# Optimization experiments

Hardware: AMD Instinct MI355X
Metric: run time of the kernel (lower is better)

## Reference

```python
import jax, jax.numpy as jnp
import numpy as np

B, S, D, H = 4, 2048, 1024, 16
HD = D // H  # head dim = 64


def setup_inputs() -> dict:
    key = jax.random.key(0)
    ks = jax.random.split(key, 10)
    scale = 1.0 / np.sqrt(D)
    return {
        "query": jax.random.normal(ks[0], (B, S, D), jnp.float32),
        "key": jax.random.normal(ks[1], (B, S, D), jnp.float32),
        "value": jax.random.normal(ks[2], (B, S, D), jnp.float32),
        "mask": jnp.zeros((B, 1, 1, S), jnp.bool_),  # True = masked out
        "Wq": jax.random.normal(ks[3], (D, D), jnp.float32) * scale,
        "bq": jnp.zeros((D,), jnp.float32),
        "Wk": jax.random.normal(ks[4], (D, D), jnp.float32) * scale,
        "bk": jnp.zeros((D,), jnp.float32),
        "Wv": jax.random.normal(ks[5], (D, D), jnp.float32) * scale,
        "bv": jnp.zeros((D,), jnp.float32),
    }


def reference(query, key, value, mask, Wq, bq, Wk, bk, Wv, bv):
    # QKV projections, then split heads: [B,S,D] -> [B,H,S,HD]
    def split_heads(x):
        return x.reshape(B, S, H, HD).transpose(0, 2, 1, 3)

    q = split_heads(query @ Wq + bq)
    k = split_heads(key @ Wk + bk)
    v = split_heads(value @ Wv + bv)

    inv_sqrt_d = jnp.float32(1.0 / np.sqrt(HD))
    scores = jnp.einsum("bhqd,bhkd->bhqk", q, k) * inv_sqrt_d  # [B,H,S,S]
    # Source semantics: tf.where(mask == False, scores, -inf) -> mask True is masked
    scores = jnp.where(mask, -jnp.inf, scores)
    attn = jax.nn.softmax(scores, axis=-1)
    out = jnp.einsum("bhqk,bhkd->bhqd", attn, v)  # [B,H,S,HD]
    # merge heads back to [B,S,D]; source forward() omits the output projection
    return out.transpose(0, 2, 1, 3).reshape(B, S, D)
```

## Files before the change

kernel.cpp:

```cpp
#include <hip/hip_runtime.h>
#include <hip/hip_bf16.h>
#include <stdint.h>


#define Bn 4
#define Sn 2048
#define Dn 1024
#define Hn 16
#define HDn 64

typedef __attribute__((ext_vector_type(8))) short short8;
typedef __attribute__((ext_vector_type(4))) float f32x4;
typedef __attribute__((ext_vector_type(4))) int i32x4;

__device__ __forceinline__ unsigned short f2b(float f) {
  __hip_bfloat16 h = __float2bfloat16(f);
  return __builtin_bit_cast(unsigned short, h);
}

__device__ __forceinline__ float fexp2(float x) {
#if __has_builtin(__builtin_amdgcn_exp2f)
  return __builtin_amdgcn_exp2f(x);
#else
  float r;
  asm("v_exp_f32 %0, %1" : "=v"(r) : "v"(x));
  return r;
#endif
}

__device__ __forceinline__ uint32_t cvtpk(float lo, float hi) {
  uint32_t r;
  asm("v_cvt_pk_bf16_f32 %0, %1, %2" : "=v"(r) : "v"(lo), "v"(hi));
  return r;
}

__device__ __forceinline__ void gload_lds16(const void* g, void* l) {
  __builtin_amdgcn_global_load_lds(
      (const __attribute__((address_space(1))) unsigned int*)(uintptr_t)g,
      (__attribute__((address_space(3))) unsigned int*)(uint32_t)(uintptr_t)l,
      16, 0, 0);
}

__global__ __launch_bounds__(256) void wt_kernel(const float* __restrict__ W,
                                                 unsigned short* __restrict__ Wt) {
  __shared__ float tile[32][33];
  const int k0 = blockIdx.x * 32, n0 = blockIdx.y * 32;
  const int tx = threadIdx.x, ty = threadIdx.y;
  #pragma unroll
  for (int j = 0; j < 32; j += 8)
    tile[ty + j][tx] = W[(size_t)(k0 + ty + j) * Dn + n0 + tx];
  __syncthreads();
  #pragma unroll
  for (int j = 0; j < 32; j += 8)
    Wt[(size_t)(n0 + ty + j) * Dn + k0 + tx] = f2b(tile[tx][ty + j]);
}

__global__ __launch_bounds__(256) void proj_gemm(const float* __restrict__ X,
                                                 const unsigned short* __restrict__ Wt,
                                                 const float* __restrict__ bias,
                                                 unsigned short* __restrict__ out,
                                                 int vt_mode) {
  __shared__ __align__(16) unsigned short Asm[128 * 32];
  __shared__ __align__(16) unsigned short Bsm[128 * 32];
  const int tid = threadIdx.x;
  const int wave = tid >> 6, lane = tid & 63;
  const int c = lane & 15, g = lane >> 4;
  const int m0 = blockIdx.x * 128, n0 = blockIdx.y * 128;
  const int wm = (wave >> 1) * 64, wn = (wave & 1) * 64;

  f32x4 acc[4][4];
  #pragma unroll
  for (int i = 0; i < 4; i++)
    #pragma unroll
    for (int j = 0; j < 4; j++) acc[i][j] = (f32x4){0.f, 0.f, 0.f, 0.f};

  for (int kt = 0; kt < Dn / 32; ++kt) {
    const int k0 = kt * 32;
    #pragma unroll
    for (int iss = 0; iss < 2; ++iss) {
      int idx = iss * 256 + tid;
      int r = idx >> 2, c8 = idx & 3;
      gload_lds16(Wt + (size_t)(n0 + r) * Dn + k0 + c8 * 8, &Bsm[idx * 8]);
    }
    #pragma unroll
    for (int iss = 0; iss < 2; ++iss) {
      int idx = iss * 256 + tid;
      int r = idx >> 2, c8 = idx & 3;
      const float* src = X + (size_t)(m0 + r) * Dn + k0 + c8 * 8;
      float4 v0 = *(const float4*)src;
      float4 v1 = *(const float4*)(src + 4);
      short8 pk;
      pk[0] = (short)f2b(v0.x); pk[1] = (short)f2b(v0.y);
      pk[2] = (short)f2b(v0.z); pk[3] = (short)f2b(v0.w);
      pk[4] = (short)f2b(v1.x); pk[5] = (short)f2b(v1.y);
      pk[6] = (short)f2b(v1.z); pk[7] = (short)f2b(v1.w);
      *(short8*)&Asm[idx * 8] = pk;
    }
    __syncthreads();

    short8 af[4], bfr[4];
    #pragma unroll
    for (int mf = 0; mf < 4; ++mf)
      af[mf] = *(const short8*)&Asm[(wm + mf * 16 + c) * 32 + g * 8];
    #pragma unroll
    for (int nf = 0; nf < 4; ++nf)
      bfr[nf] = *(const short8*)&Bsm[(wn + nf * 16 + c) * 32 + g * 8];
    #pragma unroll
    for (int mf = 0; mf < 4; ++mf)
      #pragma unroll
      for (int nf = 0; nf < 4; ++nf)
        acc[mf][nf] = __builtin_amdgcn_mfma_f32_16x16x32_bf16(af[mf], bfr[nf], acc[mf][nf], 0, 0, 0);
    __syncthreads();
  }

  #pragma unroll
  for (int mf = 0; mf < 4; ++mf) {
    #pragma unroll
    for (int nf = 0; nf < 4; ++nf) {
      #pragma unroll
      for (int i = 0; i < 4; ++i) {
        int row = m0 + wm + mf * 16 + g * 4 + i;
        int col = n0 + wn + nf * 16 + c;
        float v = acc[mf][nf][i] + bias[col];
        int bb = row >> 11, srow = row & 2047;
        int hh = col >> 6, hd = col & 63;
        size_t o;
        if (!vt_mode)
          o = (((size_t)bb * Hn + hh) * Sn + srow) * HDn + hd;
        else
          o = (((size_t)bb * Hn + hh) * HDn + hd) * Sn + srow;
        out[o] = f2b(v);
      }
    }
  }
}

__global__ __launch_bounds__(256) void attn_kernel(const unsigned short* __restrict__ Qg,
                                                   const unsigned short* __restrict__ Kg,
                                                   const unsigned short* __restrict__ Vtg,
                                                   const uint8_t* __restrict__ maskg,
                                                   float* __restrict__ out) {
  __shared__ __align__(16) unsigned short Ksm[2][64 * 64];
  __shared__ __align__(16) unsigned short Vsm[2][64 * 64];
  __shared__ __align__(16) uint32_t Plds[4][16 * 32];
  __shared__ __align__(16) float biasLds[Sn];

  const int b = blockIdx.z, h = blockIdx.y;
  const int q0 = blockIdx.x * 64;
  const int tid = threadIdx.x;
  const int wave = tid >> 6, lane = tid & 63;
  const int c = lane & 15, g = lane >> 4;
  const int cs = c & 7;
  const int bh = b * Hn + h;

  const unsigned short* kbase = Kg + (size_t)bh * Sn * HDn;
  const unsigned short* vbase = Vtg + (size_t)bh * HDn * Sn;

  const unsigned short* qptr = Qg + ((size_t)bh * Sn + q0 + wave * 16 + c) * HDn;
  const short8 qf0 = *(const short8*)(qptr + g * 8);
  const short8 qf1 = *(const short8*)(qptr + 32 + g * 8);

  auto stage = [&](int t, int buf) {
    const int kv0 = t * 64;
    #pragma unroll
    for (int iss = 0; iss < 2; ++iss) {
      int idx = iss * 256 + tid;
      int r = idx >> 3, c8 = idx & 7;
      int c8s = c8 ^ (r & 7);
      gload_lds16(kbase + (size_t)(kv0 + r) * HDn + c8s * 8, &Ksm[buf][idx * 8]);
      gload_lds16(vbase + (size_t)r * Sn + kv0 + c8s * 8, &Vsm[buf][idx * 8]);
    }
  };

  stage(0, 0);

  {
    const uint8_t* mb = maskg + (size_t)b * Sn;
    uint2 w = *(const uint2*)(mb + tid * 8);
    float4 f0, f1;
    f0.x = (w.x & 0x000000ffu) ? -1e30f : 0.f;
    f0.y = (w.x & 0x0000ff00u) ? -1e30f : 0.f;
    f0.z = (w.x & 0x00ff0000u) ? -1e30f : 0.f;
    f0.w = (w.x & 0xff000000u) ? -1e30f : 0.f;
    f1.x = (w.y & 0x000000ffu) ? -1e30f : 0.f;
    f1.y = (w.y & 0x0000ff00u) ? -1e30f : 0.f;
    f1.z = (w.y & 0x00ff0000u) ? -1e30f : 0.f;
    f1.w = (w.y & 0xff000000u) ? -1e30f : 0.f;
    *(float4*)&biasLds[tid * 8] = f0;
    *(float4*)&biasLds[tid * 8 + 4] = f1;
  }
  __syncthreads();

  f32x4 O[4];
  #pragma unroll
  for (int i = 0; i < 4; i++) O[i] = (f32x4){0.f, 0.f, 0.f, 0.f};
  float m = -INFINITY, l = 0.f;

  const float SCALE = 0.125f * 1.44269504088896340736f;
  uint32_t* pw = &Plds[wave][0];

  for (int t = 0; t < Sn / 64; ++t) {
    const int cur = t & 1;
    const int kv0 = t * 64;
    if (t < Sn / 64 - 1) stage(t + 1, cur ^ 1);

    f32x4 s[4];
    #pragma unroll
    for (int cf = 0; cf < 4; ++cf) {
      const unsigned short* krow = &Ksm[cur][(cf * 16 + c) * 64];
      short8 kb0 = *(const short8*)&krow[((0 + g) ^ cs) * 8];
      short8 kb1 = *(const short8*)&krow[((4 + g) ^ cs) * 8];
      s[cf] = (f32x4){0.f, 0.f, 0.f, 0.f};
      s[cf] = __builtin_amdgcn_mfma_f32_16x16x32_bf16(kb0, qf0, s[cf], 0, 0, 0);
      s[cf] = __builtin_amdgcn_mfma_f32_16x16x32_bf16(kb1, qf1, s[cf], 0, 0, 0);
    }

    #pragma unroll
    for (int cf = 0; cf < 4; ++cf) {
      f32x4 bv = *(const f32x4*)&biasLds[kv0 + cf * 16 + g * 4];
      #pragma unroll
      for (int i = 0; i < 4; i++) s[cf][i] = s[cf][i] * SCALE + bv[i];
    }

    float pm = s[0][0];
    #pragma unroll
    for (int cf = 0; cf < 4; ++cf)
      #pragma unroll
      for (int i = 0; i < 4; i++) pm = fmaxf(pm, s[cf][i]);
    pm = fmaxf(pm, __shfl_xor(pm, 16, 64));
    pm = fmaxf(pm, __shfl_xor(pm, 32, 64));

    if (__any(pm > m + 8.0f)) {
      float mn = fmaxf(m, pm);
      float sf = fexp2(m - mn);
      m = mn;
      l *= sf;
      #pragma unroll
      for (int hf = 0; hf < 4; ++hf)
        #pragma unroll
        for (int i = 0; i < 4; i++) O[hf][i] *= sf;
    }

    float rs = 0.f;
    #pragma unroll
    for (int cf = 0; cf < 4; ++cf)
      #pragma unroll
      for (int i = 0; i < 4; i++) {
        float p = fexp2(s[cf][i] - m);
        s[cf][i] = p;
        rs += p;
      }
    rs += __shfl_xor(rs, 16, 64);
    rs += __shfl_xor(rs, 32, 64);
    l += rs;

    #pragma unroll
    for (int cf = 0; cf < 4; ++cf) {
      uint32_t w0 = cvtpk(s[cf][0], s[cf][1]);
      uint32_t w1 = cvtpk(s[cf][2], s[cf][3]);
      int base = (cf * 8 + g * 2) ^ (cs << 2);
      pw[c * 32 + base] = w0;
      pw[c * 32 + base + 1] = w1;
    }
    short8 pb0 = *(const short8*)&pw[c * 32 + ((g * 4) ^ (cs << 2))];
    short8 pb1 = *(const short8*)&pw[c * 32 + ((16 + g * 4) ^ (cs << 2))];
    #pragma unroll
    for (int hf = 0; hf < 4; ++hf) {
      const unsigned short* vrow = &Vsm[cur][(hf * 16 + c) * 64];
      short8 va0 = *(const short8*)&vrow[((0 + g) ^ cs) * 8];
      short8 va1 = *(const short8*)&vrow[((4 + g) ^ cs) * 8];
      O[hf] = __builtin_amdgcn_mfma_f32_16x16x32_bf16(va0, pb0, O[hf], 0, 0, 0);
      O[hf] = __builtin_amdgcn_mfma_f32_16x16x32_bf16(va1, pb1, O[hf], 0, 0, 0);
    }
    __syncthreads();
  }

  const float inv = 1.0f / l;
  const int q = q0 + wave * 16 + c;
  float* op = out + ((size_t)b * Sn + q) * Dn + h * HDn;
  #pragma unroll
  for (int hf = 0; hf < 4; ++hf) {
    float4 st;
    st.x = O[hf][0] * inv;
    st.y = O[hf][1] * inv;
    st.z = O[hf][2] * inv;
    st.w = O[hf][3] * inv;
    *(float4*)&op[hf * 16 + g * 4] = st;
  }
}

extern "C" void kernel_launch(void* const* d_in, const int* in_sizes, int n_in,
                              void* d_out, int out_size, void* d_ws, size_t ws_size,
                              hipStream_t stream) {
  (void)in_sizes; (void)n_in; (void)out_size; (void)ws_size;
  const float* query = (const float*)d_in[0];
  const float* key   = (const float*)d_in[1];
  const float* value = (const float*)d_in[2];
  const uint8_t* mask = (const uint8_t*)d_in[3];
  const float* Wq = (const float*)d_in[4];
  const float* bq = (const float*)d_in[5];
  const float* Wk = (const float*)d_in[6];
  const float* bk = (const float*)d_in[7];
  const float* Wv = (const float*)d_in[8];
  const float* bv = (const float*)d_in[9];
  float* out = (float*)d_out;

  unsigned short* wtq = (unsigned short*)d_ws;
  unsigned short* wtk = wtq + (size_t)Dn * Dn;
  unsigned short* wtv = wtk + (size_t)Dn * Dn;
  unsigned short* Qb  = wtv + (size_t)Dn * Dn;
  unsigned short* Kb  = Qb + (size_t)Bn * Sn * Dn;
  unsigned short* Vtb = Kb + (size_t)Bn * Sn * Dn;

  dim3 tb(32, 8);
  dim3 tg(Dn / 32, Dn / 32);
  wt_kernel<<<tg, tb, 0, stream>>>(Wq, wtq);
  wt_kernel<<<tg, tb, 0, stream>>>(Wk, wtk);
  wt_kernel<<<tg, tb, 0, stream>>>(Wv, wtv);

  dim3 gg(Bn * Sn / 128, Dn / 128);
  proj_gemm<<<gg, 256, 0, stream>>>(query, wtq, bq, Qb, 0);
  proj_gemm<<<gg, 256, 0, stream>>>(key,   wtk, bk, Kb, 0);
  proj_gemm<<<gg, 256, 0, stream>>>(value, wtv, bv, Vtb, 1);

  dim3 ag(Sn / 64, Hn, Bn);
  attn_kernel<<<ag, 256, 0, stream>>>(Qb, Kb, Vtb, mask, out);
}
```

Measured before the change: 424.6 us.

## Batch QKV launches, fold softmax scale into Q, skip bias for unmasked tiles

Merges the three weight-transpose launches and the three projection GEMMs into single launches indexed by blockIdx.z, so each stage fills the GPU with one larger grid. The softmax scale (1/sqrt(d)·log2 e) is folded into the Q projection epilogue, and bf16 conversion uses packed cvt instructions. In the attention loop a per-64-key-tile mask flag lets fully unmasked tiles skip the bias add, and the row-max is computed as a shallower reduction tree. Rounding Q to bf16 after scaling slightly changes numerics, and the flag check adds a small LDS read per tile.

```diff
diff --git a/kernel.cpp b/kernel.cpp
--- a/kernel.cpp
+++ b/kernel.cpp
@@ -8,6 +8,7 @@
 #define Dn 1024
 #define Hn 16
 #define HDn 64
+#define QSCALE (0.125f * 1.44269504088896340736f)
 
 typedef __attribute__((ext_vector_type(8))) short short8;
 typedef __attribute__((ext_vector_type(4))) float f32x4;
@@ -41,9 +42,16 @@
       16, 0, 0);
 }
 
-__global__ __launch_bounds__(256) void wt_kernel(const float* __restrict__ W,
-                                                 unsigned short* __restrict__ Wt) {
+__global__ __launch_bounds__(256) void wt3_kernel(const float* __restrict__ Wq,
+                                                  const float* __restrict__ Wk,
+                                                  const float* __restrict__ Wv,
+                                                  unsigned short* __restrict__ wtq,
+                                                  unsigned short* __restrict__ wtk,
+                                                  unsigned short* __restrict__ wtv) {
   __shared__ float tile[32][33];
+  const int z = blockIdx.z;
+  const float* W = z == 0 ? Wq : (z == 1 ? Wk : Wv);
+  unsigned short* Wt = z == 0 ? wtq : (z == 1 ? wtk : wtv);
   const int k0 = blockIdx.x * 32, n0 = blockIdx.y * 32;
   const int tx = threadIdx.x, ty = threadIdx.y;
   #pragma unroll
@@ -55,13 +63,28 @@
     Wt[(size_t)(n0 + ty + j) * Dn + k0 + tx] = f2b(tile[tx][ty + j]);
 }
 
-__global__ __launch_bounds__(256) void proj_gemm(const float* __restrict__ X,
-                                                 const unsigned short* __restrict__ Wt,
-                                                 const float* __restrict__ bias,
-                                                 unsigned short* __restrict__ out,
-                                                 int vt_mode) {
+__global__ __launch_bounds__(256) void proj3_gemm(const float* __restrict__ Xq,
+                                                  const float* __restrict__ Xk,
+                                                  const float* __restrict__ Xv,
+                                                  const unsigned short* __restrict__ wtq,
+                                                  const unsigned short* __restrict__ wtk,
+                                                  const unsigned short* __restrict__ wtv,
+                                                  const float* __restrict__ bq,
+                                                  const float* __restrict__ bk,
+                                                  const float* __restrict__ bv,
+                                                  unsigned short* __restrict__ Qb,
+                                                  unsigned short* __restrict__ Kb,
+                                                  unsigned short* __restrict__ Vtb) {
   __shared__ __align__(16) unsigned short Asm[128 * 32];
   __shared__ __align__(16) unsigned short Bsm[128 * 32];
+  const int z = blockIdx.z;
+  const float* X = z == 0 ? Xq : (z == 1 ? Xk : Xv);
+  const unsigned short* Wt = z == 0 ? wtq : (z == 1 ? wtk : wtv);
+  const float* bias = z == 0 ? bq : (z == 1 ? bk : bv);
+  unsigned short* out = z == 0 ? Qb : (z == 1 ? Kb : Vtb);
+  const float osc = z == 0 ? QSCALE : 1.0f;
+  const int vt_mode = (z == 2);
+
   const int tid = threadIdx.x;
   const int wave = tid >> 6, lane = tid & 63;
   const int c = lane & 15, g = lane >> 4;
@@ -89,12 +112,12 @@
       const float* src = X + (size_t)(m0 + r) * Dn + k0 + c8 * 8;
       float4 v0 = *(const float4*)src;
       float4 v1 = *(const float4*)(src + 4);
-      short8 pk;
-      pk[0] = (short)f2b(v0.x); pk[1] = (short)f2b(v0.y);
-      pk[2] = (short)f2b(v0.z); pk[3] = (short)f2b(v0.w);
-      pk[4] = (short)f2b(v1.x); pk[5] = (short)f2b(v1.y);
-      pk[6] = (short)f2b(v1.z); pk[7] = (short)f2b(v1.w);
-      *(short8*)&Asm[idx * 8] = pk;
+      i32x4 pk;
+      pk[0] = (int)cvtpk(v0.x, v0.y);
+      pk[1] = (int)cvtpk(v0.z, v0.w);
+      pk[2] = (int)cvtpk(v1.x, v1.y);
+      pk[3] = (int)cvtpk(v1.z, v1.w);
+      *(i32x4*)&Asm[idx * 8] = pk;
     }
     __syncthreads();
 
@@ -121,7 +144,7 @@
       for (int i = 0; i < 4; ++i) {
         int row = m0 + wm + mf * 16 + g * 4 + i;
         int col = n0 + wn + nf * 16 + c;
-        float v = acc[mf][nf][i] + bias[col];
+        float v = (acc[mf][nf][i] + bias[col]) * osc;
         int bb = row >> 11, srow = row & 2047;
         int hh = col >> 6, hd = col & 63;
         size_t o;
@@ -144,6 +167,7 @@
   __shared__ __align__(16) unsigned short Vsm[2][64 * 64];
   __shared__ __align__(16) uint32_t Plds[4][16 * 32];
   __shared__ __align__(16) float biasLds[Sn];
+  __shared__ int flagsLds[Sn / 64];
 
   const int b = blockIdx.z, h = blockIdx.y;
   const int q0 = blockIdx.x * 64;
@@ -155,6 +179,7 @@
 
   const unsigned short* kbase = Kg + (size_t)bh * Sn * HDn;
   const unsigned short* vbase = Vtg + (size_t)bh * HDn * Sn;
+  const uint8_t* mb = maskg + (size_t)b * Sn;
 
   const unsigned short* qptr = Qg + ((size_t)bh * Sn + q0 + wave * 16 + c) * HDn;
   const short8 qf0 = *(const short8*)(qptr + g * 8);
@@ -174,8 +199,14 @@
 
   stage(0, 0);
 
+  if (tid < Sn / 64) {
+    const uint4* mp = (const uint4*)(mb + tid * 64);
+    uint4 a = mp[0], d = mp[1], e = mp[2], f = mp[3];
+    uint32_t o = a.x | a.y | a.z | a.w | d.x | d.y | d.z | d.w |
+                 e.x | e.y | e.z | e.w | f.x | f.y | f.z | f.w;
+    flagsLds[tid] = (o != 0) ? 1 : 0;
+  }
   {
-    const uint8_t* mb = maskg + (size_t)b * Sn;
     uint2 w = *(const uint2*)(mb + tid * 8);
     float4 f0, f1;
     f0.x = (w.x & 0x000000ffu) ? -1e30f : 0.f;
@@ -196,7 +227,6 @@
   for (int i = 0; i < 4; i++) O[i] = (f32x4){0.f, 0.f, 0.f, 0.f};
   float m = -INFINITY, l = 0.f;
 
-  const float SCALE = 0.125f * 1.44269504088896340736f;
   uint32_t* pw = &Plds[wave][0];
 
   for (int t = 0; t < Sn / 64; ++t) {
@@ -215,18 +245,23 @@
       s[cf] = __builtin_amdgcn_mfma_f32_16x16x32_bf16(kb1, qf1, s[cf], 0, 0, 0);
     }
 
-    #pragma unroll
-    for (int cf = 0; cf < 4; ++cf) {
-      f32x4 bv = *(const f32x4*)&biasLds[kv0 + cf * 16 + g * 4];
-      #pragma unroll
-      for (int i = 0; i < 4; i++) s[cf][i] = s[cf][i] * SCALE + bv[i];
-    }
-
-    float pm = s[0][0];
-    #pragma unroll
-    for (int cf = 0; cf < 4; ++cf)
-      #pragma unroll
-      for (int i = 0; i < 4; i++) pm = fmaxf(pm, s[cf][i]);
+    if (flagsLds[t]) {
+      #pragma unroll
+      for (int cf = 0; cf < 4; ++cf) {
+        f32x4 bv = *(const f32x4*)&biasLds[kv0 + cf * 16 + g * 4];
+        #pragma unroll
+        for (int i = 0; i < 4; i++) s[cf][i] += bv[i];
+      }
+    }
+
+    float t0 = fmaxf(fmaxf(s[0][0], s[0][1]), s[0][2]);
+    float t1 = fmaxf(fmaxf(s[0][3], s[1][0]), s[1][1]);
+    float t2 = fmaxf(fmaxf(s[1][2], s[1][3]), s[2][0]);
+    float t3 = fmaxf(fmaxf(s[2][1], s[2][2]), s[2][3]);
+    float t4 = fmaxf(fmaxf(s[3][0], s[3][1]), s[3][2]);
+    float u0 = fmaxf(fmaxf(t0, t1), s[3][3]);
+    float u1 = fmaxf(fmaxf(t2, t3), t4);
+    float pm = fmaxf(u0, u1);
     pm = fmaxf(pm, __shfl_xor(pm, 16, 64));
     pm = fmaxf(pm, __shfl_xor(pm, 32, 64));
 
@@ -313,15 +348,12 @@
   unsigned short* Vtb = Kb + (size_t)Bn * Sn * Dn;
 
   dim3 tb(32, 8);
-  dim3 tg(Dn / 32, Dn / 32);
-  wt_kernel<<<tg, tb, 0, stream>>>(Wq, wtq);
-  wt_kernel<<<tg, tb, 0, stream>>>(Wk, wtk);
-  wt_kernel<<<tg, tb, 0, stream>>>(Wv, wtv);
-
-  dim3 gg(Bn * Sn / 128, Dn / 128);
-  proj_gemm<<<gg, 256, 0, stream>>>(query, wtq, bq, Qb, 0);
-  proj_gemm<<<gg, 256, 0, stream>>>(key,   wtk, bk, Kb, 0);
-  proj_gemm<<<gg, 256, 0, stream>>>(value, wtv, bv, Vtb, 1);
+  dim3 tg(Dn / 32, Dn / 32, 3);
+  wt3_kernel<<<tg, tb, 0, stream>>>(Wq, Wk, Wv, wtq, wtk, wtv);
+
+  dim3 gg(Bn * Sn / 128, Dn / 128, 3);
+  proj3_gemm<<<gg, 256, 0, stream>>>(query, key, value, wtq, wtk, wtv,
+                                     bq, bk, bv, Qb, Kb, Vtb);
 
   dim3 ag(Sn / 64, Hn, Bn);
   attn_kernel<<<ag, 256, 0, stream>>>(Qb, Kb, Vtb, mask, out);
```

After: 387.2 us. -8.8%, faster.
